# Optimization experiments

Measured on AMD Instinct MI355X. Metric: run time of the kernel, lower is better.

Reference implementation:

```python
import jax, jax.numpy as jnp
import numpy as np

N, F_IN, H1, H2, LC, HEADS, MAX_K = 2048, 768, 512, 256, 256, 2, 512

leaky = lambda x: jax.nn.leaky_relu(x, 0.01)

def setup_inputs() -> dict:
    key = jax.random.key(0)
    ks = jax.random.split(key, 32)
    def w(k, shape):
        return jax.random.normal(k, shape, dtype=jnp.float32) * 0.05
    def sparse_adj(k):
        m = (jax.random.uniform(k, (N, N)) < 0.01).astype(jnp.float32)
        return m / (m.sum(axis=1, keepdims=True) + 1.0)
    inp = {
        'ns_emb': jax.random.normal(ks[0], (N, F_IN), dtype=jnp.float32),
        'adj': sparse_adj(ks[1]),
        'adj_prior': sparse_adj(ks[2]),
        'condition': jax.random.normal(ks[3], (1, LC, F_IN), dtype=jnp.float32),
        'labels': (jax.random.uniform(ks[4], (N, N)) < 0.01).astype(jnp.float32),
        'eps': jax.random.normal(ks[5], (N, H2), dtype=jnp.float32),
        'W_map': w(ks[6], (F_IN, H2)),
    }
    i = 7
    for pref in ('post', 'prior'):
        inp[pref + '_W_hid'] = w(ks[i], (F_IN, H1)); i += 1
        inp[pref + '_Wq'] = w(ks[i], (H1, H1)); i += 1
        inp[pref + '_Wk'] = w(ks[i], (F_IN, H1)); i += 1
        inp[pref + '_Wv'] = w(ks[i], (F_IN, H1)); i += 1
        inp[pref + '_Wo'] = w(ks[i], (H1, H1)); i += 1
        inp[pref + '_W_mu'] = w(ks[i], (H1, H2)); i += 1
        inp[pref + '_W_var'] = w(ks[i], (H1, H2)); i += 1
    return inp

def gcn(x, W, adj):
    # support = Linear(x); out = act(adj @ act(support))
    s = x @ W
    return leaky(adj @ leaky(s))

def mha(q_in, cond, Wq, Wk, Wv, Wo):
    # q_in: [N, H1]; cond: [Lc, F_IN]; 2-head scaled dot-product attention
    n, d = q_in.shape
    lc = cond.shape[0]
    dh = d // HEADS
    q = (q_in @ Wq).reshape(n, HEADS, dh).transpose(1, 0, 2)
    k = (cond @ Wk).reshape(lc, HEADS, dh).transpose(1, 0, 2)
    v = (cond @ Wv).reshape(lc, HEADS, dh).transpose(1, 0, 2)
    scores = jnp.einsum('hnd,hmd->hnm', q, k) / np.float32(np.sqrt(dh))
    attn = jax.nn.softmax(scores, axis=-1)
    o = jnp.einsum('hnm,hmd->hnd', attn, v).transpose(1, 0, 2).reshape(n, d)
    return o @ Wo

def encode(ns_emb, adj, cond, W_hid, Wq, Wk, Wv, Wo, W_mu, W_var):
    hidden = gcn(ns_emb, W_hid, adj)
    hidden = mha(hidden, cond, Wq, Wk, Wv, Wo)
    return gcn(hidden, W_mu, adj), gcn(hidden, W_var, adj)

def rel_represent(ns_emb, adj_triu, W_map):
    # ns_matrix[a*N+b] = f(ns_emb)[a] + f(ns_emb)[b]; gather topk rows without
    # materializing the [N^2, H2] outer-sum tensor.
    n = ns_emb.shape[0]
    ns2 = leaky(ns_emb @ W_map)                      # [N, H2]
    _, idx = jax.lax.top_k(adj_triu.reshape(-1), MAX_K)
    a, b = idx // n, idx % n
    selected = ns2[a] + ns2[b]                       # [MAX_K, H2]
    rel_num = (n * n - n) / 2.0
    rel_mask = jnp.arange(MAX_K) >= rel_num          # all False here
    return selected, rel_mask

def loss_function(preds, labels, mu_pair, lv_pair):
    n = labels.shape[0]
    s = labels.sum()
    pos_weight = (n * n - s + n) / (s - n + 0.01)
    norm = (n * n) / (n * n - s + n)
    # BCE-with-logits applied to sigmoid outputs, faithful to the original
    bce = -(pos_weight * labels * jax.nn.log_sigmoid(preds)
            + (1.0 - labels) * jax.nn.log_sigmoid(-preds))
    recons = norm * bce.mean()
    (mu_po, mu_pr), (lv_po, lv_pr) = mu_pair, lv_pair
    kld = 0.5 / n * jnp.mean(jnp.sum(
        (mu_pr - mu_po) ** 2 / jnp.exp(lv_pr) + jnp.exp(lv_po - lv_pr)
        - 1.0 - (lv_po - lv_pr), axis=1))
    return recons, kld

def reference(ns_emb, adj, adj_prior, condition, labels, eps, W_map,
              post_W_hid, post_Wq, post_Wk, post_Wv, post_Wo, post_W_mu, post_W_var,
              prior_W_hid, prior_Wq, prior_Wk, prior_Wv, prior_Wo, prior_W_mu, prior_W_var):
    cond = condition[0]
    mu, logvar = encode(ns_emb, adj, cond, post_W_hid, post_Wq, post_Wk,
                        post_Wv, post_Wo, post_W_mu, post_W_var)
    mu_pr, logvar_pr = encode(ns_emb, adj_prior, cond, prior_W_hid, prior_Wq,
                              prior_Wk, prior_Wv, prior_Wo, prior_W_mu, prior_W_var)
    z = eps * jnp.exp(0.5 * logvar) + mu             # reparameterize (train)
    recover_adj = jax.nn.sigmoid(z @ z.T)            # InnerProductDecoder
    adj_triu = jnp.triu(recover_adj, k=1)
    relations, rel_mask = rel_represent(ns_emb, adj_triu, W_map)
    recons, kld = loss_function(recover_adj, labels, (mu, mu_pr), (logvar, logvar_pr))
    return relations, rel_mask, recons, kld
```

## Files before the change

### kernel.cpp

```cpp
#include <hip/hip_runtime.h>
#include <math.h>
#include <stdint.h>


namespace {

constexpr int NN   = 2048;
constexpr int FIN  = 768;
constexpr int H1D  = 512;
constexpr int H2D  = 256;
constexpr int LCD  = 256;
constexpr int TOPK = 512;
constexpr int TOTE = NN * NN;
constexpr int CAP  = 96;
constexpr unsigned ONEB = 0x3F800000u;

struct SelState {
  unsigned cnt1, T, r, tieRow, tieRem, Ithr, cTotal, pad;
  double sum1, sum0, labSum, kldSum;
};

struct Slot  { const float* A; const float* B; float* C;
               int lda, ldb, ldc, nshift, act; float scale; };
struct Launch{ Slot s[8]; int zend[8]; };
struct EB { const float* adj[2]; int* cnt[2]; int* col[2]; float* val[2]; };
struct SB { const int* cnt[2]; const int* col[2]; const float* val[2];
            const float* S[2]; float* out[2]; };

__device__ __forceinline__ float leaky(float v) { return v >= 0.f ? v : 0.01f * v; }

template<int TRANSB>
__global__ __launch_bounds__(256)
void mega_gemm(Launch P, int K)
{
  const int G = gridDim.x;
  const int bid = blockIdx.x;
  const int wg = (bid & 7) * (G >> 3) + (bid >> 3);
  int z = 0, start = 0;
  #pragma unroll
  for (int i = 0; i < 7; ++i)
    if (wg >= P.zend[i]) { z = i + 1; start = P.zend[i]; }
  Slot sl = P.s[0];
  #pragma unroll
  for (int i = 1; i < 8; ++i) if (z == i) sl = P.s[i];
  const int local = wg - start;
  const int by = local >> sl.nshift;
  const int bx = local & ((1 << sl.nshift) - 1);

  __shared__ float As[2][16][68];
  __shared__ float Bs[2][16][68];
  const int t  = threadIdx.x;
  const int bm = by * 64, bn = bx * 64;
  const int lr = t >> 2, lq = t & 3;
  const int bkr = t >> 4, bnq = t & 15;
  const int tx = t & 15, ty = t >> 4;
  const float* Aptr = sl.A + (long long)(bm + lr) * sl.lda + lq * 4;
  const float* Bt   = sl.B + (long long)(bn + lr) * sl.ldb + lq * 4;
  const float* Bn   = sl.B + (long long)bkr * sl.ldb + bn + bnq * 4;
  float acc[4][4] = {};
  float4 av, bv;

  auto loadg = [&](int k0) {
    av = *(const float4*)(Aptr + k0);
    bv = TRANSB ? *(const float4*)(Bt + k0)
                : *(const float4*)(Bn + (long long)k0 * sl.ldb);
  };
  auto stage = [&](int bf) {
    As[bf][lq*4+0][lr]=av.x; As[bf][lq*4+1][lr]=av.y; As[bf][lq*4+2][lr]=av.z; As[bf][lq*4+3][lr]=av.w;
    if (TRANSB) {
      Bs[bf][lq*4+0][lr]=bv.x; Bs[bf][lq*4+1][lr]=bv.y; Bs[bf][lq*4+2][lr]=bv.z; Bs[bf][lq*4+3][lr]=bv.w;
    } else {
      *(float4*)&Bs[bf][bkr][bnq*4] = bv;
    }
  };
  auto compute = [&](int bf) {
    #pragma unroll
    for (int kk = 0; kk < 16; ++kk) {
      float4 a = *(const float4*)&As[bf][kk][ty*4];
      float4 b = *(const float4*)&Bs[bf][kk][tx*4];
      acc[0][0]+=a.x*b.x; acc[0][1]+=a.x*b.y; acc[0][2]+=a.x*b.z; acc[0][3]+=a.x*b.w;
      acc[1][0]+=a.y*b.x; acc[1][1]+=a.y*b.y; acc[1][2]+=a.y*b.z; acc[1][3]+=a.y*b.w;
      acc[2][0]+=a.z*b.x; acc[2][1]+=a.z*b.y; acc[2][2]+=a.z*b.z; acc[2][3]+=a.z*b.w;
      acc[3][0]+=a.w*b.x; acc[3][1]+=a.w*b.y; acc[3][2]+=a.w*b.z; acc[3][3]+=a.w*b.w;
    }
  };

  loadg(0); stage(0); __syncthreads();
  int cur = 0;
  for (int k0 = 16; k0 < K; k0 += 16) {
    loadg(k0);
    compute(cur);
    stage(cur ^ 1);
    __syncthreads();
    cur ^= 1;
  }
  compute(cur);

  #pragma unroll
  for (int i = 0; i < 4; ++i) {
    float4 v;
    float* vp = &v.x;
    #pragma unroll
    for (int j = 0; j < 4; ++j) {
      float q = acc[i][j] * sl.scale;
      if (sl.act == 1) q = leaky(q);
      else if (sl.act == 2) q = 1.f / (1.f + expf(-q));
      vp[j] = q;
    }
    *(float4*)&sl.C[(long long)(bm + ty*4 + i) * sl.ldc + bn + tx*4] = v;
  }
}

__global__ __launch_bounds__(256)
void zzt_fused(const float* __restrict__ zv, const float* __restrict__ labels,
               float* __restrict__ radj, SelState* st, unsigned* __restrict__ rowTies)
{
  const int bx = blockIdx.x, by = blockIdx.y;
  if (bx < by) return;
  __shared__ float As[2][32][68];
  __shared__ float Bs[2][32][68];
  __shared__ unsigned rt[64];
  __shared__ float red[256];
  const int t = threadIdx.x;
  if (t < 64) rt[t] = 0;
  const int bm = by * 64, bn = bx * 64;
  const int lr = t >> 2, lq = t & 3;
  const int tx = t & 15, ty = t >> 4;
  const float* Ap = zv + (long long)(bm + lr) * 256 + lq * 4;
  const float* Bp = zv + (long long)(bn + lr) * 256 + lq * 4;
  float acc[4][4] = {};
  float4 a0, a1, b0, b1;

  auto loadg = [&](int k0) {
    a0 = *(const float4*)(Ap + k0); a1 = *(const float4*)(Ap + k0 + 16);
    b0 = *(const float4*)(Bp + k0); b1 = *(const float4*)(Bp + k0 + 16);
  };
  auto stage = [&](int bf) {
    As[bf][lq*4+0][lr]=a0.x; As[bf][lq*4+1][lr]=a0.y; As[bf][lq*4+2][lr]=a0.z; As[bf][lq*4+3][lr]=a0.w;
    As[bf][lq*4+16][lr]=a1.x; As[bf][lq*4+17][lr]=a1.y; As[bf][lq*4+18][lr]=a1.z; As[bf][lq*4+19][lr]=a1.w;
    Bs[bf][lq*4+0][lr]=b0.x; Bs[bf][lq*4+1][lr]=b0.y; Bs[bf][lq*4+2][lr]=b0.z; Bs[bf][lq*4+3][lr]=b0.w;
    Bs[bf][lq*4+16][lr]=b1.x; Bs[bf][lq*4+17][lr]=b1.y; Bs[bf][lq*4+18][lr]=b1.z; Bs[bf][lq*4+19][lr]=b1.w;
  };
  auto compute = [&](int bf) {
    #pragma unroll
    for (int kk = 0; kk < 32; ++kk) {
      float4 a = *(const float4*)&As[bf][kk][ty*4];
      float4 b = *(const float4*)&Bs[bf][kk][tx*4];
      acc[0][0]+=a.x*b.x; acc[0][1]+=a.x*b.y; acc[0][2]+=a.x*b.z; acc[0][3]+=a.x*b.w;
      acc[1][0]+=a.y*b.x; acc[1][1]+=a.y*b.y; acc[1][2]+=a.y*b.z; acc[1][3]+=a.y*b.w;
      acc[2][0]+=a.z*b.x; acc[2][1]+=a.z*b.y; acc[2][2]+=a.z*b.z; acc[2][3]+=a.z*b.w;
      acc[3][0]+=a.w*b.x; acc[3][1]+=a.w*b.y; acc[3][2]+=a.w*b.z; acc[3][3]+=a.w*b.w;
    }
  };

  loadg(0); stage(0); __syncthreads();
  int cur = 0;
  for (int k0 = 32; k0 < 256; k0 += 32) {
    loadg(k0);
    compute(cur);
    stage(cur ^ 1);
    __syncthreads();
    cur ^= 1;
  }
  compute(cur);

  float o[4][4];
  #pragma unroll
  for (int i = 0; i < 4; ++i)
    #pragma unroll
    for (int j = 0; j < 4; ++j)
      o[i][j] = 1.f / (1.f + expf(-acc[i][j]));

  #pragma unroll
  for (int i = 0; i < 4; ++i)
    *(float4*)&radj[(long long)(bm + ty*4 + i) * NN + bn + tx*4] =
        make_float4(o[i][0], o[i][1], o[i][2], o[i][3]);
  if (bx > by) {
    #pragma unroll
    for (int j = 0; j < 4; ++j)
      *(float4*)&radj[(long long)(bn + tx*4 + j) * NN + bm + ty*4] =
          make_float4(o[0][j], o[1][j], o[2][j], o[3][j]);
  }

  float s1 = 0.f, s0 = 0.f, slb = 0.f;
  unsigned myc1 = 0;
  unsigned c1row[4] = {0, 0, 0, 0};
  #pragma unroll
  for (int i = 0; i < 4; ++i) {
    const int gr = bm + ty*4 + i;
    float4 lbp = *(const float4*)&labels[(long long)gr * NN + bn + tx*4];
    const float* lp = &lbp.x;
    #pragma unroll
    for (int j = 0; j < 4; ++j) {
      const int gc = bn + tx*4 + j;
      float p = o[i][j];
      float e = expf(-p), l1p = log1pf(e);
      float lb = lp[j];
      s1 += lb * l1p;
      s0 += (1.f - lb) * (p + l1p);
      slb += lb;
      if ((bx > by || gc > gr) && __float_as_uint(p) == ONEB) { c1row[i]++; myc1++; }
    }
  }
  if (bx > by) {
    #pragma unroll
    for (int j = 0; j < 4; ++j) {
      float4 lbm = *(const float4*)&labels[(long long)(bn + tx*4 + j) * NN + bm + ty*4];
      const float* lp = &lbm.x;
      #pragma unroll
      for (int i = 0; i < 4; ++i) {
        float p = o[i][j];
        float e = expf(-p), l1p = log1pf(e);
        float lb = lp[i];
        s1 += lb * l1p;
        s0 += (1.f - lb) * (p + l1p);
        slb += lb;
      }
    }
  }
  #pragma unroll
  for (int i = 0; i < 4; ++i)
    if (c1row[i]) atomicAdd(&rt[ty*4 + i], c1row[i]);

  __syncthreads();
  red[t] = s1; __syncthreads();
  for (int s = 128; s > 0; s >>= 1) { if (t < s) red[t] += red[t + s]; __syncthreads(); }
  if (t == 0) atomicAdd(&st->sum1, (double)red[0]);
  __syncthreads();
  red[t] = s0; __syncthreads();
  for (int s = 128; s > 0; s >>= 1) { if (t < s) red[t] += red[t + s]; __syncthreads(); }
  if (t == 0) atomicAdd(&st->sum0, (double)red[0]);
  __syncthreads();
  red[t] = slb; __syncthreads();
  for (int s = 128; s > 0; s >>= 1) { if (t < s) red[t] += red[t + s]; __syncthreads(); }
  if (t == 0) atomicAdd(&st->labSum, (double)red[0]);
  __syncthreads();
  red[t] = (float)myc1; __syncthreads();
  for (int s = 128; s > 0; s >>= 1) { if (t < s) red[t] += red[t + s]; __syncthreads(); }
  if (t == 0 && red[0] > 0.f) atomicAdd(&st->cnt1, (unsigned)red[0]);
  if (t < 64 && rt[t]) atomicAdd(&rowTies[bm + t], rt[t]);
}

__global__ __launch_bounds__(64)
void build_ell(EB eb)
{
  const int b = blockIdx.y, row = blockIdx.x, lane = threadIdx.x;
  const float* adj = eb.adj[b];
  int base = 0;
  for (int c0 = 0; c0 < NN; c0 += 64) {
    float v = adj[(long long)row * NN + c0 + lane];
    unsigned long long m = __ballot(v != 0.0f);
    if (v != 0.0f) {
      int pos = base + __popcll(m & ((1ull << lane) - 1ull));
      if (pos < CAP) { eb.col[b][row * CAP + pos] = c0 + lane; eb.val[b][row * CAP + pos] = v; }
    }
    base += __popcll(m);
  }
  if (lane == 0) eb.cnt[b][row] = base > CAP ? CAP : base;
}

__global__ __launch_bounds__(256)
void spmm_leaky(SB sb)
{
  const int b = blockIdx.y, row = blockIdx.x, t = threadIdx.x;
  __shared__ int   sc[CAP];
  __shared__ float sv[CAP];
  __shared__ int   n;
  if (t == 0) n = sb.cnt[b][row];
  if (t < CAP) { sc[t] = sb.col[b][row * CAP + t]; sv[t] = sb.val[b][row * CAP + t]; }
  __syncthreads();
  const int m = n;
  const float* S = sb.S[b];
  float a0 = 0.f, a1 = 0.f;
  for (int i = 0; i < m; ++i) {
    const float* Sr = S + (long long)sc[i] * 512;
    float v = sv[i];
    a0 += v * Sr[t];
    a1 += v * Sr[t + 256];
  }
  sb.out[b][(long long)row * 512 + t]       = leaky(a0);
  sb.out[b][(long long)row * 512 + t + 256] = leaky(a1);
}

__global__ __launch_bounds__(256)
void softmax256(float* __restrict__ x)
{
  const int row = blockIdx.x * 4 + (threadIdx.x >> 6);
  const int l = threadIdx.x & 63;
  float4 v = *(float4*)&x[(long long)row * 256 + l * 4];
  float m = fmaxf(fmaxf(v.x, v.y), fmaxf(v.z, v.w));
  for (int s = 32; s; s >>= 1) m = fmaxf(m, __shfl_xor(m, s));
  float e0 = expf(v.x - m), e1 = expf(v.y - m), e2 = expf(v.z - m), e3 = expf(v.w - m);
  float sm = e0 + e1 + e2 + e3;
  for (int s = 32; s; s >>= 1) sm += __shfl_xor(sm, s);
  float inv = 1.f / sm;
  *(float4*)&x[(long long)row * 256 + l * 4] = make_float4(e0*inv, e1*inv, e2*inv, e3*inv);
}

__global__ __launch_bounds__(256)
void z_kld(const float* __restrict__ eps, const float* __restrict__ mpo,
           const float* __restrict__ mpr, float* __restrict__ z, SelState* st)
{
  __shared__ float red[256];
  const int row = blockIdx.x, c = threadIdx.x;
  float mu = mpo[row * 512 + c], lv = mpo[row * 512 + 256 + c];
  z[row * 256 + c] = eps[row * 256 + c] * expf(0.5f * lv) + mu;
  float mu2 = mpr[row * 512 + c], lv2 = mpr[row * 512 + 256 + c];
  float d = mu2 - mu, dl = lv - lv2;
  red[c] = d * d * expf(-lv2) + expf(dl) - 1.f - dl;
  __syncthreads();
  for (int s = 128; s > 0; s >>= 1) { if (c < s) red[c] += red[c + s]; __syncthreads(); }
  if (c == 0) atomicAdd(&st->kldSum, (double)red[0]);
}

__global__ __launch_bounds__(1024)
void select_kernel(const float* __restrict__ radj, SelState* st, unsigned* __restrict__ rowTies)
{
  const int tid = threadIdx.x;
  if (st->cnt1 >= (unsigned)TOPK) {
    if (tid == 0) { st->T = ONEB; st->r = TOPK; }
    return;
  }
  __shared__ unsigned hist[256];
  __shared__ unsigned prefix_s, rem_s;
  unsigned prefix = 0, rem = TOPK;
  for (int pass = 0; pass < 4; ++pass) {
    const int shift = 24 - 8 * pass;
    const unsigned mask = pass ? (0xFFFFFFFFu << (32 - 8 * pass)) : 0u;
    if (tid < 256) hist[tid] = 0;
    __syncthreads();
    for (int idx = tid; idx < TOTE; idx += 1024) {
      int i = idx >> 11, j = idx & 2047;
      if (j <= i) continue;
      unsigned b = __float_as_uint(radj[idx]);
      if ((b & mask) == prefix) atomicAdd(&hist[(b >> shift) & 255], 1u);
    }
    __syncthreads();
    if (tid == 0) {
      unsigned cg = 0;
      for (int bb = 255; bb >= 0; --bb) {
        unsigned c = hist[bb];
        if (cg + c >= rem) { prefix |= ((unsigned)bb) << shift; rem -= cg; break; }
        cg += c;
      }
      prefix_s = prefix; rem_s = rem;
    }
    __syncthreads();
    prefix = prefix_s; rem = rem_s;
  }
  if (tid == 0) { st->T = prefix; st->r = rem; }
  for (int r = tid; r < NN; r += 1024) rowTies[r] = 0;
  __syncthreads();
  for (int idx = tid; idx < TOTE; idx += 1024) {
    int i = idx >> 11, j = idx & 2047;
    if (j <= i) continue;
    if (__float_as_uint(radj[idx]) == prefix) atomicAdd(&rowTies[i], 1u);
  }
}

__global__ __launch_bounds__(256)
void cut_row(const unsigned* __restrict__ rowTies, SelState* st)
{
  __shared__ unsigned ps[256];
  const int t = threadIdx.x;
  unsigned loc[8], s = 0;
  for (int i = 0; i < 8; ++i) { loc[i] = rowTies[t * 8 + i]; s += loc[i]; }
  ps[t] = s; __syncthreads();
  for (int sh = 1; sh < 256; sh <<= 1) {
    unsigned v = (t >= sh) ? ps[t - sh] : 0; __syncthreads();
    ps[t] += v; __syncthreads();
  }
  const unsigned r = st->r;
  const unsigned exc = ps[t] - s;
  if (r > exc && r <= ps[t]) {
    unsigned cum = exc;
    for (int i = 0; i < 8; ++i) {
      if (r <= cum + loc[i]) { st->tieRow = t * 8 + i; st->tieRem = r - cum; break; }
      cum += loc[i];
    }
  }
}

__global__ __launch_bounds__(64)
void find_col(const float* __restrict__ radj, SelState* st)
{
  const int R = (int)st->tieRow;
  const unsigned rem = st->tieRem, T = st->T;
  unsigned base = 0;
  for (int c0 = R + 1; c0 < NN; c0 += 64) {
    const int c = c0 + (int)threadIdx.x;
    bool f = (c < NN) && (__float_as_uint(radj[(long long)R * NN + c]) == T);
    unsigned long long m = __ballot(f);
    unsigned cnt = (unsigned)__popcll(m);
    if (base + cnt >= rem) {
      if (f) {
        unsigned rank = (unsigned)__popcll(m & ((1ull << threadIdx.x) - 1ull)) + 1u;
        if (base + rank == rem) st->Ithr = (unsigned)(R * NN + c);
      }
      return;
    }
    base += cnt;
  }
}

__global__ __launch_bounds__(256)
void collect_kernel(const float* __restrict__ radj, SelState* st,
                    unsigned* __restrict__ cand_bits, unsigned* __restrict__ cand_idx)
{
  const int row = blockIdx.x;
  const unsigned T = st->T, It = st->Ithr;
  for (int c = row + 1 + threadIdx.x; c < NN; c += 256) {
    int idx = row * NN + c;
    unsigned b = __float_as_uint(radj[idx]);
    if (b > T || (b == T && (unsigned)idx <= It)) {
      unsigned p = atomicAdd(&st->cTotal, 1u);
      if (p < (unsigned)TOPK) { cand_bits[p] = b; cand_idx[p] = (unsigned)idx; }
    }
  }
}

__global__ __launch_bounds__(512)
void rank_sort(const unsigned* __restrict__ cand_bits,
               const unsigned* __restrict__ cand_idx, unsigned* __restrict__ ord)
{
  __shared__ unsigned vb[512], vi[512];
  const int t = threadIdx.x;
  vb[t] = cand_bits[t]; vi[t] = cand_idx[t];
  __syncthreads();
  unsigned b = vb[t], id = vi[t];
  int rank = 0;
  for (int u = 0; u < 512; ++u)
    rank += (vb[u] > b) || (vb[u] == b && vi[u] < id);
  ord[rank] = id;
}

__global__ __launch_bounds__(256)
void gather_rel(const unsigned* __restrict__ ord, const float* __restrict__ ns2,
                float* __restrict__ out)
{
  const int r = blockIdx.x, c = threadIdx.x;
  unsigned id = ord[r];
  int a = id >> 11, b = id & 2047;
  out[r * 256 + c] = ns2[a * 256 + c] + ns2[b * 256 + c];
}

__global__ __launch_bounds__(512)
void finalize_kernel(const SelState* st, float* __restrict__ out)
{
  const int t = threadIdx.x;
  out[TOPK * H2D + t] = 0.0f;
  if (t == 0) {
    double s   = st->labSum;
    double nn  = (double)NN * NN;
    double pw  = (nn - s + NN) / (s - NN + 0.01);
    double nrm = nn / (nn - s + NN);
    out[TOPK * H2D + TOPK + 0] = (float)(nrm * (pw * st->sum1 + st->sum0) / nn);
    out[TOPK * H2D + TOPK + 1] = (float)(0.5 * st->kldSum / nn);
  }
}

}

extern "C" void kernel_launch(void* const* d_in, const int* in_sizes, int n_in,
                              void* d_out, int out_size, void* d_ws, size_t ws_size,
                              hipStream_t stream)
{
  (void)in_sizes; (void)n_in; (void)out_size; (void)ws_size;
  const float* ns_emb    = (const float*)d_in[0];
  const float* adj       = (const float*)d_in[1];
  const float* adj_prior = (const float*)d_in[2];
  const float* cond      = (const float*)d_in[3];
  const float* labels    = (const float*)d_in[4];
  const float* eps       = (const float*)d_in[5];
  const float* W_map     = (const float*)d_in[6];
  const float* Wb[2][7];
  for (int k = 0; k < 14; ++k) Wb[k / 7][k % 7] = (const float*)d_in[7 + k];
  float* out = (float*)d_out;

  char* w = (char*)d_ws;
  SelState* st      = (SelState*)w;          w += 256;
  unsigned* rowTies = (unsigned*)w;          w += NN * 4;
  unsigned* cand_bits = (unsigned*)w;        w += TOPK * 4;
  unsigned* cand_idx  = (unsigned*)w;        w += TOPK * 4;
  unsigned* ord       = (unsigned*)w;        w += TOPK * 4;
  w = (char*)(((uintptr_t)w + 255) & ~(uintptr_t)255);
  int* ellCnt[2]; int* ellCol[2]; float* ellVal[2];
  for (int b = 0; b < 2; ++b) {
    ellCnt[b] = (int*)w;   w += NN * 4;
    ellCol[b] = (int*)w;   w += (size_t)NN * CAP * 4;
    ellVal[b] = (float*)w; w += (size_t)NN * CAP * 4;
  }
  const long long NNH1 = (long long)NN * H1D;
  const long long LCH  = (long long)LCD * H1D;
  float* AR = (float*)w;  w += (size_t)(6 * NNH1 + 4 * LCH) * 4;
  float* mulv[2];
  mulv[0] = (float*)w;    w += (size_t)NNH1 * 4;
  mulv[1] = (float*)w;    w += (size_t)NNH1 * 4;
  float* zb  = (float*)w; w += (size_t)NN * H2D * 4;
  float* ns2 = (float*)w; w += (size_t)NN * H2D * 4;

  float* S[2]  = { AR,          AR + NNH1 };
  float* Q[2]  = { AR,          AR + NNH1 };
  float* H[2]  = { AR + 2*NNH1, AR + 3*NNH1 };
  float* O[2]  = { AR + 2*NNH1, AR + 3*NNH1 };
  float* Kb[2] = { AR + 4*NNH1,         AR + 4*NNH1 + LCH };
  float* Vb[2] = { AR + 4*NNH1 + 2*LCH, AR + 4*NNH1 + 3*LCH };
  float* SC    =   AR + 4*NNH1 + 4*LCH;
  float* T2[2] = { SC,          SC + NNH1 };
  float* H2[2] = { AR,          AR + NNH1 };
  float* radj  =   AR;

  hipMemsetAsync(st, 0, 256 + NN * 4, stream);

  {
    EB eb{};
    eb.adj[0] = adj; eb.adj[1] = adj_prior;
    for (int b = 0; b < 2; ++b) { eb.cnt[b]=ellCnt[b]; eb.col[b]=ellCol[b]; eb.val[b]=ellVal[b]; }
    build_ell<<<dim3(NN, 2), 64, 0, stream>>>(eb);
  }

  auto mkslot = [](const float* A, const float* B, float* C, int lda, int ldb, int ldc,
                   int nshift, int act, float scale) {
    Slot s; s.A=A; s.B=B; s.C=C; s.lda=lda; s.ldb=ldb; s.ldc=ldc;
    s.nshift=nshift; s.act=act; s.scale=scale; return s;
  };

  {
    Launch P{};
    P.s[0] = mkslot(ns_emb, Wb[0][0], S[0], FIN, H1D, H1D, 3, 1, 1.f);
    P.s[1] = mkslot(ns_emb, Wb[1][0], S[1], FIN, H1D, H1D, 3, 1, 1.f);
    P.s[2] = mkslot(cond,   Wb[0][2], Kb[0], FIN, H1D, H1D, 3, 0, 1.f);
    P.s[3] = mkslot(cond,   Wb[1][2], Kb[1], FIN, H1D, H1D, 3, 0, 1.f);
    P.s[4] = mkslot(cond,   Wb[0][3], Vb[0], FIN, H1D, H1D, 3, 0, 1.f);
    P.s[5] = mkslot(cond,   Wb[1][3], Vb[1], FIN, H1D, H1D, 3, 0, 1.f);
    P.s[6] = mkslot(ns_emb, W_map,    ns2,  FIN, H2D, H2D, 2, 1, 1.f);
    int ze[8] = {256, 512, 544, 576, 608, 640, 768, 768};
    for (int i = 0; i < 8; ++i) P.zend[i] = ze[i];
    mega_gemm<0><<<dim3(768), 256, 0, stream>>>(P, FIN);
  }
  {
    SB sb{};
    for (int br = 0; br < 2; ++br) { sb.cnt[br]=ellCnt[br]; sb.col[br]=ellCol[br];
      sb.val[br]=ellVal[br]; sb.S[br]=S[br]; sb.out[br]=H[br]; }
    spmm_leaky<<<dim3(NN, 2), 256, 0, stream>>>(sb);
  }
  {
    Launch P{};
    P.s[0] = mkslot(H[0], Wb[0][1], Q[0], H1D, H1D, H1D, 3, 0, 1.f);
    P.s[1] = mkslot(H[1], Wb[1][1], Q[1], H1D, H1D, H1D, 3, 0, 1.f);
    int ze[8] = {256, 512, 512, 512, 512, 512, 512, 512};
    for (int i = 0; i < 8; ++i) P.zend[i] = ze[i];
    mega_gemm<0><<<dim3(512), 256, 0, stream>>>(P, H1D);
  }
  {
    Launch P{};
    for (int br = 0; br < 2; ++br) for (int hd = 0; hd < 2; ++hd) {
      int z = br * 2 + hd;
      P.s[z] = mkslot(Q[br] + hd*256, Kb[br] + hd*256, SC + (long long)z*NN*256,
                      H1D, H1D, 256, 2, 0, 0.0625f);
    }
    int ze[8] = {128, 256, 384, 512, 512, 512, 512, 512};
    for (int i = 0; i < 8; ++i) P.zend[i] = ze[i];
    mega_gemm<1><<<dim3(512), 256, 0, stream>>>(P, 256);
  }
  softmax256<<<dim3(NN), 256, 0, stream>>>(SC);
  {
    Launch P{};
    for (int br = 0; br < 2; ++br) for (int hd = 0; hd < 2; ++hd) {
      int z = br * 2 + hd;
      P.s[z] = mkslot(SC + (long long)z*NN*256, Vb[br] + hd*256, O[br] + hd*256,
                      256, H1D, H1D, 2, 0, 1.f);
    }
    int ze[8] = {128, 256, 384, 512, 512, 512, 512, 512};
    for (int i = 0; i < 8; ++i) P.zend[i] = ze[i];
    mega_gemm<0><<<dim3(512), 256, 0, stream>>>(P, 256);
  }
  {
    Launch P{};
    P.s[0] = mkslot(O[0], Wb[0][4], H2[0], H1D, H1D, H1D, 3, 0, 1.f);
    P.s[1] = mkslot(O[1], Wb[1][4], H2[1], H1D, H1D, H1D, 3, 0, 1.f);
    int ze[8] = {256, 512, 512, 512, 512, 512, 512, 512};
    for (int i = 0; i < 8; ++i) P.zend[i] = ze[i];
    mega_gemm<0><<<dim3(512), 256, 0, stream>>>(P, H1D);
  }
  {
    Launch P{};
    for (int br = 0; br < 2; ++br) {
      P.s[br]   = mkslot(H2[br], Wb[br][5], T2[br],       H1D, H2D, H1D, 2, 1, 1.f);
      P.s[2+br] = mkslot(H2[br], Wb[br][6], T2[br] + H2D, H1D, H2D, H1D, 2, 1, 1.f);
    }
    int ze[8] = {128, 256, 384, 512, 512, 512, 512, 512};
    for (int i = 0; i < 8; ++i) P.zend[i] = ze[i];
    mega_gemm<0><<<dim3(512), 256, 0, stream>>>(P, H1D);
  }
  {
    SB sb{};
    for (int br = 0; br < 2; ++br) { sb.cnt[br]=ellCnt[br]; sb.col[br]=ellCol[br];
      sb.val[br]=ellVal[br]; sb.S[br]=T2[br]; sb.out[br]=mulv[br]; }
    spmm_leaky<<<dim3(NN, 2), 256, 0, stream>>>(sb);
  }

  z_kld<<<dim3(NN), 256, 0, stream>>>(eps, mulv[0], mulv[1], zb, st);
  zzt_fused<<<dim3(32, 32), 256, 0, stream>>>(zb, labels, radj, st, rowTies);

  select_kernel<<<dim3(1), 1024, 0, stream>>>(radj, st, rowTies);
  cut_row<<<dim3(1), 256, 0, stream>>>(rowTies, st);
  find_col<<<dim3(1), 64, 0, stream>>>(radj, st);
  collect_kernel<<<dim3(NN), 256, 0, stream>>>(radj, st, cand_bits, cand_idx);
  rank_sort<<<dim3(1), 512, 0, stream>>>(cand_bits, cand_idx, ord);
  gather_rel<<<dim3(TOPK), 256, 0, stream>>>(ord, ns2, out);
  finalize_kernel<<<dim3(1), 512, 0, stream>>>(st, out);
}
```

Before: 503.0 us.

## Split-K the attention GEMMs, fuse partial sums, merge selection and gather kernels

The Q, QK^T, PV and output-projection GEMMs are split along K into two halves, doubling the number of workgroups. The next consumer (the A-load of the following GEMM, or softmax) adds the two partial results, which needs larger scratch buffers. The three selection kernels (select, cut_row, find_col) become one, and the gather and finalize kernels are merged to cut launches. The zzt kernel's K tile shrinks from 32 to 16, trading less shared memory for more loop iterations and barriers.

```diff
diff --git a/kernel.cpp b/kernel.cpp
--- a/kernel.cpp
+++ b/kernel.cpp
@@ -1,6 +1,7 @@
 #include <hip/hip_runtime.h>
 #include <math.h>
 #include <stdint.h>
+#include <initializer_list>
 
 
 namespace {
@@ -13,6 +14,7 @@
 constexpr int TOPK = 512;
 constexpr int TOTE = NN * NN;
 constexpr int CAP  = 96;
+constexpr int NNQ  = NN * 256;
 constexpr unsigned ONEB = 0x3F800000u;
 
 struct SelState {
@@ -20,16 +22,16 @@
   double sum1, sum0, labSum, kldSum;
 };
 
-struct Slot  { const float* A; const float* B; float* C;
+struct Slot  { const float* A; const float* A2; const float* B; float* C;
                int lda, ldb, ldc, nshift, act; float scale; };
 struct Launch{ Slot s[8]; int zend[8]; };
 struct EB { const float* adj[2]; int* cnt[2]; int* col[2]; float* val[2]; };
 struct SB { const int* cnt[2]; const int* col[2]; const float* val[2];
-            const float* S[2]; float* out[2]; };
+            const float* S[2]; const float* S2[2]; float* out[2]; int asum; };
 
 __device__ __forceinline__ float leaky(float v) { return v >= 0.f ? v : 0.01f * v; }
 
-template<int TRANSB>
+template<int TRANSB, int ASUM>
 __global__ __launch_bounds__(256)
 void mega_gemm(Launch P, int K)
 {
@@ -54,14 +56,19 @@
   const int lr = t >> 2, lq = t & 3;
   const int bkr = t >> 4, bnq = t & 15;
   const int tx = t & 15, ty = t >> 4;
-  const float* Aptr = sl.A + (long long)(bm + lr) * sl.lda + lq * 4;
-  const float* Bt   = sl.B + (long long)(bn + lr) * sl.ldb + lq * 4;
-  const float* Bn   = sl.B + (long long)bkr * sl.ldb + bn + bnq * 4;
+  const float* Aptr  = sl.A + (long long)(bm + lr) * sl.lda + lq * 4;
+  const float* A2ptr = ASUM ? (sl.A2 + (long long)(bm + lr) * sl.lda + lq * 4) : (const float*)0;
+  const float* Bt    = sl.B + (long long)(bn + lr) * sl.ldb + lq * 4;
+  const float* Bn    = sl.B + (long long)bkr * sl.ldb + bn + bnq * 4;
   float acc[4][4] = {};
   float4 av, bv;
 
   auto loadg = [&](int k0) {
     av = *(const float4*)(Aptr + k0);
+    if (ASUM) {
+      float4 w = *(const float4*)(A2ptr + k0);
+      av.x += w.x; av.y += w.y; av.z += w.z; av.w += w.w;
+    }
     bv = TRANSB ? *(const float4*)(Bt + k0)
                 : *(const float4*)(Bn + (long long)k0 * sl.ldb);
   };
@@ -117,8 +124,8 @@
 {
   const int bx = blockIdx.x, by = blockIdx.y;
   if (bx < by) return;
-  __shared__ float As[2][32][68];
-  __shared__ float Bs[2][32][68];
+  __shared__ float As[2][16][68];
+  __shared__ float Bs[2][16][68];
   __shared__ unsigned rt[64];
   __shared__ float red[256];
   const int t = threadIdx.x;
@@ -129,21 +136,19 @@
   const float* Ap = zv + (long long)(bm + lr) * 256 + lq * 4;
   const float* Bp = zv + (long long)(bn + lr) * 256 + lq * 4;
   float acc[4][4] = {};
-  float4 a0, a1, b0, b1;
+  float4 a0, b0;
 
   auto loadg = [&](int k0) {
-    a0 = *(const float4*)(Ap + k0); a1 = *(const float4*)(Ap + k0 + 16);
-    b0 = *(const float4*)(Bp + k0); b1 = *(const float4*)(Bp + k0 + 16);
+    a0 = *(const float4*)(Ap + k0);
+    b0 = *(const float4*)(Bp + k0);
   };
   auto stage = [&](int bf) {
     As[bf][lq*4+0][lr]=a0.x; As[bf][lq*4+1][lr]=a0.y; As[bf][lq*4+2][lr]=a0.z; As[bf][lq*4+3][lr]=a0.w;
-    As[bf][lq*4+16][lr]=a1.x; As[bf][lq*4+17][lr]=a1.y; As[bf][lq*4+18][lr]=a1.z; As[bf][lq*4+19][lr]=a1.w;
     Bs[bf][lq*4+0][lr]=b0.x; Bs[bf][lq*4+1][lr]=b0.y; Bs[bf][lq*4+2][lr]=b0.z; Bs[bf][lq*4+3][lr]=b0.w;
-    Bs[bf][lq*4+16][lr]=b1.x; Bs[bf][lq*4+17][lr]=b1.y; Bs[bf][lq*4+18][lr]=b1.z; Bs[bf][lq*4+19][lr]=b1.w;
   };
   auto compute = [&](int bf) {
     #pragma unroll
-    for (int kk = 0; kk < 32; ++kk) {
+    for (int kk = 0; kk < 16; ++kk) {
       float4 a = *(const float4*)&As[bf][kk][ty*4];
       float4 b = *(const float4*)&Bs[bf][kk][tx*4];
       acc[0][0]+=a.x*b.x; acc[0][1]+=a.x*b.y; acc[0][2]+=a.x*b.z; acc[0][3]+=a.x*b.w;
@@ -155,7 +160,7 @@
 
   loadg(0); stage(0); __syncthreads();
   int cur = 0;
-  for (int k0 = 32; k0 < 256; k0 += 32) {
+  for (int k0 = 16; k0 < 256; k0 += 16) {
     loadg(k0);
     compute(cur);
     stage(cur ^ 1);
@@ -270,31 +275,43 @@
   if (t < CAP) { sc[t] = sb.col[b][row * CAP + t]; sv[t] = sb.val[b][row * CAP + t]; }
   __syncthreads();
   const int m = n;
-  const float* S = sb.S[b];
+  const float* S  = sb.S[b];
+  const float* S2 = sb.S2[b];
   float a0 = 0.f, a1 = 0.f;
-  for (int i = 0; i < m; ++i) {
-    const float* Sr = S + (long long)sc[i] * 512;
-    float v = sv[i];
-    a0 += v * Sr[t];
-    a1 += v * Sr[t + 256];
+  if (sb.asum) {
+    for (int i = 0; i < m; ++i) {
+      long long off = (long long)sc[i] * 512;
+      float v = sv[i];
+      a0 += v * leaky(S[off + t]       + S2[off + t]);
+      a1 += v * leaky(S[off + t + 256] + S2[off + t + 256]);
+    }
+  } else {
+    for (int i = 0; i < m; ++i) {
+      long long off = (long long)sc[i] * 512;
+      float v = sv[i];
+      a0 += v * S[off + t];
+      a1 += v * S[off + t + 256];
+    }
   }
   sb.out[b][(long long)row * 512 + t]       = leaky(a0);
   sb.out[b][(long long)row * 512 + t + 256] = leaky(a1);
 }
 
 __global__ __launch_bounds__(256)
-void softmax256(float* __restrict__ x)
-{
-  const int row = blockIdx.x * 4 + (threadIdx.x >> 6);
+void softmax256(float* __restrict__ x, const float* __restrict__ p2)
+{
+  const long long row = blockIdx.x * 4 + (threadIdx.x >> 6);
   const int l = threadIdx.x & 63;
-  float4 v = *(float4*)&x[(long long)row * 256 + l * 4];
+  float4 v = *(float4*)&x[row * 256 + l * 4];
+  float4 w = *(const float4*)&p2[row * 256 + l * 4];
+  v.x += w.x; v.y += w.y; v.z += w.z; v.w += w.w;
   float m = fmaxf(fmaxf(v.x, v.y), fmaxf(v.z, v.w));
   for (int s = 32; s; s >>= 1) m = fmaxf(m, __shfl_xor(m, s));
   float e0 = expf(v.x - m), e1 = expf(v.y - m), e2 = expf(v.z - m), e3 = expf(v.w - m);
   float sm = e0 + e1 + e2 + e3;
   for (int s = 32; s; s >>= 1) sm += __shfl_xor(sm, s);
   float inv = 1.f / sm;
-  *(float4*)&x[(long long)row * 256 + l * 4] = make_float4(e0*inv, e1*inv, e2*inv, e3*inv);
+  *(float4*)&x[row * 256 + l * 4] = make_float4(e0*inv, e1*inv, e2*inv, e3*inv);
 }
 
 __global__ __launch_bounds__(256)
@@ -314,93 +331,103 @@
 }
 
 __global__ __launch_bounds__(1024)
-void select_kernel(const float* __restrict__ radj, SelState* st, unsigned* __restrict__ rowTies)
+void select_all(const float* __restrict__ radj, SelState* st,
+                const unsigned* __restrict__ rowTies)
 {
   const int tid = threadIdx.x;
-  if (st->cnt1 >= (unsigned)TOPK) {
-    if (tid == 0) { st->T = ONEB; st->r = TOPK; }
-    return;
-  }
+  __shared__ unsigned rt[NN];
   __shared__ unsigned hist[256];
+  __shared__ unsigned ps[256];
+  __shared__ unsigned sT, sR, sRow, sRem;
   __shared__ unsigned prefix_s, rem_s;
-  unsigned prefix = 0, rem = TOPK;
-  for (int pass = 0; pass < 4; ++pass) {
-    const int shift = 24 - 8 * pass;
-    const unsigned mask = pass ? (0xFFFFFFFFu << (32 - 8 * pass)) : 0u;
-    if (tid < 256) hist[tid] = 0;
+
+  const bool fast = (st->cnt1 >= (unsigned)TOPK);
+  if (fast) {
+    if (tid == 0) { sT = ONEB; sR = TOPK; }
+    for (int r = tid; r < NN; r += 1024) rt[r] = rowTies[r];
+    __syncthreads();
+  } else {
+    unsigned prefix = 0, rem = TOPK;
+    for (int pass = 0; pass < 4; ++pass) {
+      const int shift = 24 - 8 * pass;
+      const unsigned mask = pass ? (0xFFFFFFFFu << (32 - 8 * pass)) : 0u;
+      if (tid < 256) hist[tid] = 0;
+      __syncthreads();
+      for (int idx = tid; idx < TOTE; idx += 1024) {
+        int i = idx >> 11, j = idx & 2047;
+        if (j <= i) continue;
+        unsigned b = __float_as_uint(radj[idx]);
+        if ((b & mask) == prefix) atomicAdd(&hist[(b >> shift) & 255], 1u);
+      }
+      __syncthreads();
+      if (tid == 0) {
+        unsigned cg = 0;
+        for (int bb = 255; bb >= 0; --bb) {
+          unsigned c = hist[bb];
+          if (cg + c >= rem) { prefix |= ((unsigned)bb) << shift; rem -= cg; break; }
+          cg += c;
+        }
+        prefix_s = prefix; rem_s = rem;
+      }
+      __syncthreads();
+      prefix = prefix_s; rem = rem_s;
+    }
+    if (tid == 0) { sT = prefix; sR = rem; }
+    for (int r = tid; r < NN; r += 1024) rt[r] = 0;
     __syncthreads();
     for (int idx = tid; idx < TOTE; idx += 1024) {
       int i = idx >> 11, j = idx & 2047;
       if (j <= i) continue;
-      unsigned b = __float_as_uint(radj[idx]);
-      if ((b & mask) == prefix) atomicAdd(&hist[(b >> shift) & 255], 1u);
+      if (__float_as_uint(radj[idx]) == prefix) atomicAdd(&rt[i], 1u);
     }
     __syncthreads();
-    if (tid == 0) {
-      unsigned cg = 0;
-      for (int bb = 255; bb >= 0; --bb) {
-        unsigned c = hist[bb];
-        if (cg + c >= rem) { prefix |= ((unsigned)bb) << shift; rem -= cg; break; }
-        cg += c;
+  }
+
+  unsigned s = 0, loc[8];
+  if (tid < 256) {
+    for (int i = 0; i < 8; ++i) { loc[i] = rt[tid * 8 + i]; s += loc[i]; }
+    ps[tid] = s;
+  }
+  __syncthreads();
+  for (int sh = 1; sh < 256; sh <<= 1) {
+    unsigned v = 0;
+    if (tid < 256 && tid >= sh) v = ps[tid - sh];
+    __syncthreads();
+    if (tid < 256 && tid >= sh) ps[tid] += v;
+    __syncthreads();
+  }
+  const unsigned r = sR;
+  if (tid < 256) {
+    const unsigned exc = ps[tid] - s;
+    if (r > exc && r <= ps[tid]) {
+      unsigned cum = exc;
+      for (int i = 0; i < 8; ++i) {
+        if (r <= cum + loc[i]) { sRow = tid * 8 + i; sRem = r - cum; break; }
+        cum += loc[i];
       }
-      prefix_s = prefix; rem_s = rem;
-    }
-    __syncthreads();
-    prefix = prefix_s; rem = rem_s;
-  }
-  if (tid == 0) { st->T = prefix; st->r = rem; }
-  for (int r = tid; r < NN; r += 1024) rowTies[r] = 0;
-  __syncthreads();
-  for (int idx = tid; idx < TOTE; idx += 1024) {
-    int i = idx >> 11, j = idx & 2047;
-    if (j <= i) continue;
-    if (__float_as_uint(radj[idx]) == prefix) atomicAdd(&rowTies[i], 1u);
-  }
-}
-
-__global__ __launch_bounds__(256)
-void cut_row(const unsigned* __restrict__ rowTies, SelState* st)
-{
-  __shared__ unsigned ps[256];
-  const int t = threadIdx.x;
-  unsigned loc[8], s = 0;
-  for (int i = 0; i < 8; ++i) { loc[i] = rowTies[t * 8 + i]; s += loc[i]; }
-  ps[t] = s; __syncthreads();
-  for (int sh = 1; sh < 256; sh <<= 1) {
-    unsigned v = (t >= sh) ? ps[t - sh] : 0; __syncthreads();
-    ps[t] += v; __syncthreads();
-  }
-  const unsigned r = st->r;
-  const unsigned exc = ps[t] - s;
-  if (r > exc && r <= ps[t]) {
-    unsigned cum = exc;
-    for (int i = 0; i < 8; ++i) {
-      if (r <= cum + loc[i]) { st->tieRow = t * 8 + i; st->tieRem = r - cum; break; }
-      cum += loc[i];
-    }
-  }
-}
-
-__global__ __launch_bounds__(64)
-void find_col(const float* __restrict__ radj, SelState* st)
-{
-  const int R = (int)st->tieRow;
-  const unsigned rem = st->tieRem, T = st->T;
-  unsigned base = 0;
-  for (int c0 = R + 1; c0 < NN; c0 += 64) {
-    const int c = c0 + (int)threadIdx.x;
-    bool f = (c < NN) && (__float_as_uint(radj[(long long)R * NN + c]) == T);
-    unsigned long long m = __ballot(f);
-    unsigned cnt = (unsigned)__popcll(m);
-    if (base + cnt >= rem) {
-      if (f) {
-        unsigned rank = (unsigned)__popcll(m & ((1ull << threadIdx.x) - 1ull)) + 1u;
-        if (base + rank == rem) st->Ithr = (unsigned)(R * NN + c);
+    }
+  }
+  __syncthreads();
+  if (tid < 64) {
+    const int R = (int)sRow;
+    const unsigned rem = sRem, T = sT;
+    unsigned base = 0;
+    for (int c0 = R + 1; c0 < NN; c0 += 64) {
+      const int c = c0 + tid;
+      bool f = (c < NN) && (__float_as_uint(radj[(long long)R * NN + c]) == T);
+      unsigned long long m = __ballot(f);
+      unsigned cnt = (unsigned)__popcll(m);
+      if (base + cnt >= rem) {
+        if (f) {
+          unsigned rank = (unsigned)__popcll(m & ((1ull << tid) - 1ull)) + 1u;
+          if (base + rank == rem) st->Ithr = (unsigned)(R * NN + c);
+        }
+        break;
       }
-      return;
-    }
-    base += cnt;
-  }
+      base += cnt;
+    }
+  }
+  if (tid == 0) { st->T = sT; st->r = sR; }
 }
 
 __global__ __launch_bounds__(256)
@@ -435,27 +462,25 @@
 }
 
 __global__ __launch_bounds__(256)
-void gather_rel(const unsigned* __restrict__ ord, const float* __restrict__ ns2,
-                float* __restrict__ out)
-{
-  const int r = blockIdx.x, c = threadIdx.x;
-  unsigned id = ord[r];
-  int a = id >> 11, b = id & 2047;
-  out[r * 256 + c] = ns2[a * 256 + c] + ns2[b * 256 + c];
-}
-
-__global__ __launch_bounds__(512)
-void finalize_kernel(const SelState* st, float* __restrict__ out)
-{
-  const int t = threadIdx.x;
-  out[TOPK * H2D + t] = 0.0f;
-  if (t == 0) {
-    double s   = st->labSum;
-    double nn  = (double)NN * NN;
-    double pw  = (nn - s + NN) / (s - NN + 0.01);
-    double nrm = nn / (nn - s + NN);
-    out[TOPK * H2D + TOPK + 0] = (float)(nrm * (pw * st->sum1 + st->sum0) / nn);
-    out[TOPK * H2D + TOPK + 1] = (float)(0.5 * st->kldSum / nn);
+void gather_fin(const unsigned* __restrict__ ord, const float* __restrict__ ns2,
+                const SelState* st, float* __restrict__ out)
+{
+  const int r = blockIdx.x, t = threadIdx.x;
+  if (r < TOPK) {
+    unsigned id = ord[r];
+    int a = id >> 11, b = id & 2047;
+    out[r * 256 + t] = ns2[a * 256 + t] + ns2[b * 256 + t];
+  } else {
+    const int half = r - TOPK;
+    out[TOPK * H2D + half * 256 + t] = 0.0f;
+    if (half == 1 && t == 0) {
+      double s   = st->labSum;
+      double nn  = (double)NN * NN;
+      double pw  = (nn - s + NN) / (s - NN + 0.01);
+      double nrm = nn / (nn - s + NN);
+      out[TOPK * H2D + TOPK + 0] = (float)(nrm * (pw * st->sum1 + st->sum0) / nn);
+      out[TOPK * H2D + TOPK + 1] = (float)(0.5 * st->kldSum / nn);
+    }
   }
 }
 
@@ -492,23 +517,26 @@
   }
   const long long NNH1 = (long long)NN * H1D;
   const long long LCH  = (long long)LCD * H1D;
-  float* AR = (float*)w;  w += (size_t)(6 * NNH1 + 4 * LCH) * 4;
+  float* AR = (float*)w;  w += (size_t)(8 * NNH1 + 4 * LCH) * 4;
   float* mulv[2];
   mulv[0] = (float*)w;    w += (size_t)NNH1 * 4;
   mulv[1] = (float*)w;    w += (size_t)NNH1 * 4;
   float* zb  = (float*)w; w += (size_t)NN * H2D * 4;
   float* ns2 = (float*)w; w += (size_t)NN * H2D * 4;
 
-  float* S[2]  = { AR,          AR + NNH1 };
-  float* Q[2]  = { AR,          AR + NNH1 };
-  float* H[2]  = { AR + 2*NNH1, AR + 3*NNH1 };
-  float* O[2]  = { AR + 2*NNH1, AR + 3*NNH1 };
-  float* Kb[2] = { AR + 4*NNH1,         AR + 4*NNH1 + LCH };
-  float* Vb[2] = { AR + 4*NNH1 + 2*LCH, AR + 4*NNH1 + 3*LCH };
-  float* SC    =   AR + 4*NNH1 + 4*LCH;
-  float* T2[2] = { SC,          SC + NNH1 };
-  float* H2[2] = { AR,          AR + NNH1 };
-  float* radj  =   AR;
+  float* A_[8];
+  for (int i = 0; i < 8; ++i) A_[i] = AR + (long long)i * NNH1;
+  float* KV = AR + 8 * NNH1;
+  float* Kb[2] = { KV,           KV + LCH };
+  float* Vb[2] = { KV + 2*LCH,   KV + 3*LCH };
+  float* S[2]   = { A_[0], A_[1] };
+  float* H[2]   = { A_[2], A_[3] };
+  float* Qp1[2] = { A_[4], A_[5] }, *Qp2[2] = { A_[6], A_[7] };
+  float* SCp1 = A_[0], *SCp2 = A_[2];
+  float* Op1[2] = { A_[4], A_[5] }, *Op2[2] = { A_[6], A_[7] };
+  float* H2p1[2] = { A_[0], A_[1] }, *H2p2[2] = { A_[2], A_[3] };
+  float* T2[2]  = { A_[4], A_[5] };
+  float* radj = A_[0];
 
   hipMemsetAsync(st, 0, 256 + NN * 4, stream);
 
@@ -519,95 +547,106 @@
     build_ell<<<dim3(NN, 2), 64, 0, stream>>>(eb);
   }
 
-  auto mkslot = [](const float* A, const float* B, float* C, int lda, int ldb, int ldc,
-                   int nshift, int act, float scale) {
-    Slot s; s.A=A; s.B=B; s.C=C; s.lda=lda; s.ldb=ldb; s.ldc=ldc;
+  auto mkslot = [](const float* A, const float* A2, const float* B, float* C,
+                   int lda, int ldb, int ldc, int nshift, int act, float scale) {
+    Slot s; s.A=A; s.A2=A2; s.B=B; s.C=C; s.lda=lda; s.ldb=ldb; s.ldc=ldc;
     s.nshift=nshift; s.act=act; s.scale=scale; return s;
   };
+  auto setz = [](Launch& P, std::initializer_list<int> ze) {
+    int i = 0, last = 0;
+    for (int v : ze) { P.zend[i++] = v; last = v; }
+    for (; i < 8; ++i) P.zend[i] = last;
+  };
 
   {
     Launch P{};
-    P.s[0] = mkslot(ns_emb, Wb[0][0], S[0], FIN, H1D, H1D, 3, 1, 1.f);
-    P.s[1] = mkslot(ns_emb, Wb[1][0], S[1], FIN, H1D, H1D, 3, 1, 1.f);
-    P.s[2] = mkslot(cond,   Wb[0][2], Kb[0], FIN, H1D, H1D, 3, 0, 1.f);
-    P.s[3] = mkslot(cond,   Wb[1][2], Kb[1], FIN, H1D, H1D, 3, 0, 1.f);
-    P.s[4] = mkslot(cond,   Wb[0][3], Vb[0], FIN, H1D, H1D, 3, 0, 1.f);
-    P.s[5] = mkslot(cond,   Wb[1][3], Vb[1], FIN, H1D, H1D, 3, 0, 1.f);
-    P.s[6] = mkslot(ns_emb, W_map,    ns2,  FIN, H2D, H2D, 2, 1, 1.f);
-    int ze[8] = {256, 512, 544, 576, 608, 640, 768, 768};
-    for (int i = 0; i < 8; ++i) P.zend[i] = ze[i];
-    mega_gemm<0><<<dim3(768), 256, 0, stream>>>(P, FIN);
+    P.s[0] = mkslot(ns_emb, 0, Wb[0][0], S[0], FIN, H1D, H1D, 3, 1, 1.f);
+    P.s[1] = mkslot(ns_emb, 0, Wb[1][0], S[1], FIN, H1D, H1D, 3, 1, 1.f);
+    P.s[2] = mkslot(cond,   0, Wb[0][2], Kb[0], FIN, H1D, H1D, 3, 0, 1.f);
+    P.s[3] = mkslot(cond,   0, Wb[1][2], Kb[1], FIN, H1D, H1D, 3, 0, 1.f);
+    P.s[4] = mkslot(cond,   0, Wb[0][3], Vb[0], FIN, H1D, H1D, 3, 0, 1.f);
+    P.s[5] = mkslot(cond,   0, Wb[1][3], Vb[1], FIN, H1D, H1D, 3, 0, 1.f);
+    P.s[6] = mkslot(ns_emb, 0, W_map,    ns2,  FIN, H2D, H2D, 2, 1, 1.f);
+    setz(P, {256, 512, 544, 576, 608, 640, 768, 768});
+    mega_gemm<0,0><<<dim3(768), 256, 0, stream>>>(P, FIN);
   }
   {
     SB sb{};
     for (int br = 0; br < 2; ++br) { sb.cnt[br]=ellCnt[br]; sb.col[br]=ellCol[br];
-      sb.val[br]=ellVal[br]; sb.S[br]=S[br]; sb.out[br]=H[br]; }
+      sb.val[br]=ellVal[br]; sb.S[br]=S[br]; sb.S2[br]=0; sb.out[br]=H[br]; }
+    sb.asum = 0;
     spmm_leaky<<<dim3(NN, 2), 256, 0, stream>>>(sb);
   }
   {
     Launch P{};
-    P.s[0] = mkslot(H[0], Wb[0][1], Q[0], H1D, H1D, H1D, 3, 0, 1.f);
-    P.s[1] = mkslot(H[1], Wb[1][1], Q[1], H1D, H1D, H1D, 3, 0, 1.f);
-    int ze[8] = {256, 512, 512, 512, 512, 512, 512, 512};
-    for (int i = 0; i < 8; ++i) P.zend[i] = ze[i];
-    mega_gemm<0><<<dim3(512), 256, 0, stream>>>(P, H1D);
+    for (int br = 0; br < 2; ++br)
+      for (int kh = 0; kh < 2; ++kh)
+        P.s[br*2+kh] = mkslot(H[br] + kh*256, 0, Wb[br][1] + kh*256*H1D,
+                              (kh ? Qp2 : Qp1)[br], H1D, H1D, H1D, 3, 0, 1.f);
+    setz(P, {256, 512, 768, 1024});
+    mega_gemm<0,0><<<dim3(1024), 256, 0, stream>>>(P, 256);
   }
   {
     Launch P{};
-    for (int br = 0; br < 2; ++br) for (int hd = 0; hd < 2; ++hd) {
-      int z = br * 2 + hd;
-      P.s[z] = mkslot(Q[br] + hd*256, Kb[br] + hd*256, SC + (long long)z*NN*256,
-                      H1D, H1D, 256, 2, 0, 0.0625f);
-    }
-    int ze[8] = {128, 256, 384, 512, 512, 512, 512, 512};
-    for (int i = 0; i < 8; ++i) P.zend[i] = ze[i];
-    mega_gemm<1><<<dim3(512), 256, 0, stream>>>(P, 256);
-  }
-  softmax256<<<dim3(NN), 256, 0, stream>>>(SC);
+    for (int br = 0; br < 2; ++br)
+      for (int hd = 0; hd < 2; ++hd)
+        for (int kh = 0; kh < 2; ++kh) {
+          int z = br*2 + hd;
+          P.s[z*2+kh] = mkslot(Qp1[br] + hd*256 + kh*128, Qp2[br] + hd*256 + kh*128,
+                               Kb[br] + hd*256 + kh*128,
+                               (kh ? SCp2 : SCp1) + (long long)z*NNQ,
+                               H1D, H1D, 256, 2, 0, 0.0625f);
+        }
+    setz(P, {128, 256, 384, 512, 640, 768, 896, 1024});
+    mega_gemm<1,1><<<dim3(1024), 256, 0, stream>>>(P, 128);
+  }
+  softmax256<<<dim3(NN), 256, 0, stream>>>(SCp1, SCp2);
   {
     Launch P{};
-    for (int br = 0; br < 2; ++br) for (int hd = 0; hd < 2; ++hd) {
-      int z = br * 2 + hd;
-      P.s[z] = mkslot(SC + (long long)z*NN*256, Vb[br] + hd*256, O[br] + hd*256,
-                      256, H1D, H1D, 2, 0, 1.f);
-    }
-    int ze[8] = {128, 256, 384, 512, 512, 512, 512, 512};
-    for (int i = 0; i < 8; ++i) P.zend[i] = ze[i];
-    mega_gemm<0><<<dim3(512), 256, 0, stream>>>(P, 256);
+    for (int br = 0; br < 2; ++br)
+      for (int hd = 0; hd < 2; ++hd)
+        for (int kh = 0; kh < 2; ++kh) {
+          int z = br*2 + hd;
+          P.s[z*2+kh] = mkslot(SCp1 + (long long)z*NNQ + kh*128, 0,
+                               Vb[br] + (long long)(kh*128)*H1D + hd*256,
+                               (kh ? Op2 : Op1)[br] + hd*256,
+                               256, H1D, H1D, 2, 0, 1.f);
+        }
+    setz(P, {128, 256, 384, 512, 640, 768, 896, 1024});
+    mega_gemm<0,0><<<dim3(1024), 256, 0, stream>>>(P, 128);
   }
   {
     Launch P{};
-    P.s[0] = mkslot(O[0], Wb[0][4], H2[0], H1D, H1D, H1D, 3, 0, 1.f);
-    P.s[1] = mkslot(O[1], Wb[1][4], H2[1], H1D, H1D, H1D, 3, 0, 1.f);
-    int ze[8] = {256, 512, 512, 512, 512, 512, 512, 512};
-    for (int i = 0; i < 8; ++i) P.zend[i] = ze[i];
-    mega_gemm<0><<<dim3(512), 256, 0, stream>>>(P, H1D);
+    for (int br = 0; br < 2; ++br)
+      for (int kh = 0; kh < 2; ++kh)
+        P.s[br*2+kh] = mkslot(Op1[br] + kh*256, Op2[br] + kh*256,
+                              Wb[br][4] + kh*256*H1D,
+                              (kh ? H2p2 : H2p1)[br], H1D, H1D, H1D, 3, 0, 1.f);
+    setz(P, {256, 512, 768, 1024});
+    mega_gemm<0,1><<<dim3(1024), 256, 0, stream>>>(P, 256);
   }
   {
     Launch P{};
     for (int br = 0; br < 2; ++br) {
-      P.s[br]   = mkslot(H2[br], Wb[br][5], T2[br],       H1D, H2D, H1D, 2, 1, 1.f);
-      P.s[2+br] = mkslot(H2[br], Wb[br][6], T2[br] + H2D, H1D, H2D, H1D, 2, 1, 1.f);
-    }
-    int ze[8] = {128, 256, 384, 512, 512, 512, 512, 512};
-    for (int i = 0; i < 8; ++i) P.zend[i] = ze[i];
-    mega_gemm<0><<<dim3(512), 256, 0, stream>>>(P, H1D);
+      P.s[br*2+0] = mkslot(H2p1[br], H2p2[br], Wb[br][5], T2[br],       H1D, H2D, H1D, 2, 1, 1.f);
+      P.s[br*2+1] = mkslot(H2p1[br], H2p2[br], Wb[br][6], T2[br] + H2D, H1D, H2D, H1D, 2, 1, 1.f);
+    }
+    setz(P, {128, 256, 384, 512});
+    mega_gemm<0,1><<<dim3(512), 256, 0, stream>>>(P, H1D);
   }
   {
     SB sb{};
     for (int br = 0; br < 2; ++br) { sb.cnt[br]=ellCnt[br]; sb.col[br]=ellCol[br];
-      sb.val[br]=ellVal[br]; sb.S[br]=T2[br]; sb.out[br]=mulv[br]; }
+      sb.val[br]=ellVal[br]; sb.S[br]=T2[br]; sb.S2[br]=0; sb.out[br]=mulv[br]; }
+    sb.asum = 0;
     spmm_leaky<<<dim3(NN, 2), 256, 0, stream>>>(sb);
   }
 
   z_kld<<<dim3(NN), 256, 0, stream>>>(eps, mulv[0], mulv[1], zb, st);
   zzt_fused<<<dim3(32, 32), 256, 0, stream>>>(zb, labels, radj, st, rowTies);
 
-  select_kernel<<<dim3(1), 1024, 0, stream>>>(radj, st, rowTies);
-  cut_row<<<dim3(1), 256, 0, stream>>>(rowTies, st);
-  find_col<<<dim3(1), 64, 0, stream>>>(radj, st);
+  select_all<<<dim3(1), 1024, 0, stream>>>(radj, st, rowTies);
   collect_kernel<<<dim3(NN), 256, 0, stream>>>(radj, st, cand_bits, cand_idx);
   rank_sort<<<dim3(1), 512, 0, stream>>>(cand_bits, cand_idx, ord);
-  gather_rel<<<dim3(TOPK), 256, 0, stream>>>(ord, ns2, out);
-  finalize_kernel<<<dim3(1), 512, 0, stream>>>(st, out);
-}
+  gather_fin<<<dim3(TOPK + 2), 256, 0, stream>>>(ord, ns2, st, out);
+}
```

After: 511.9 us. About the same (+1.8%).
